# Optimization experiments

Hardware: AMD Instinct MI355X
Metric: run time of the kernel (lower is better)

Reference implementation:

```python
import jax, jax.numpy as jnp
import numpy as np

B, C, L = 32, 128, 4096          # batch, n_channels, signal length
P, Q = 100, 20                   # n_projections, n_quantiles


def setup_inputs() -> dict:
    key = jax.random.key(0)
    k1, k2, k3, k4 = jax.random.split(key, 4)
    X = jax.random.normal(k1, (B, C, L), dtype=jnp.float32)
    # conv1d kernel of shape (P, C, 1) collapsed to (P, C)
    W = jax.random.normal(k2, (P, C), dtype=jnp.float32)
    s = 2.33 * jnp.sqrt(jnp.float32(C))
    min_vals = -s + 0.1 * jax.random.normal(k3, (P,), dtype=jnp.float32)
    max_vals = s + 0.1 * jax.random.normal(k4, (P,), dtype=jnp.float32)
    return {"X": X, "W": W, "min_vals": min_vals, "max_vals": max_vals}


def reference(X, W, min_vals, max_vals):
    # kernel-size-1 conv1d == channel projection
    a = jnp.einsum('bcl,pc->bpl', X, W)  # [B, P, L]
    fracs = jnp.arange(1, Q + 1, dtype=a.dtype) / jnp.asarray(Q + 1, a.dtype)
    thr = min_vals[None, :] + (max_vals - min_vals)[None, :] * fracs[:, None]  # [Q, P]

    def body(carry, t):  # t: [P] thresholds for one quantile
        cdf_q = jnp.mean((a < t[None, :, None]).astype(a.dtype), axis=-1)  # [B, P]
        return carry, cdf_q

    _, cdf = jax.lax.scan(body, None, thr)          # [Q, B, P]
    cdf = jnp.transpose(cdf, (1, 2, 0))             # [B, P, Q]
    return cdf.reshape(B, P * Q)
```

## Files before the change

kernel.cpp:

```cpp
#include <hip/hip_runtime.h>
#include <hip/hip_bf16.h>

#define B_    32
#define C_    128
#define L_    4096
#define P_    100
#define NPT   7
#define Q_    20
#define NBIN  21
#define HSTR  37
#define NCH   (NPT * 4)
#define CHS   512
#define TPB   1024
#define LSPAN 512

typedef short          bf16x8 __attribute__((ext_vector_type(8)));
typedef float          f32x4  __attribute__((ext_vector_type(4)));
typedef unsigned short u16x8  __attribute__((ext_vector_type(8)));

__device__ inline unsigned short f2bf(float f) {
    __hip_bfloat16 h = __float2bfloat16(f);
    unsigned short u; __builtin_memcpy(&u, &h, 2);
    return u;
}

__global__ void prep_w_kernel(const float* __restrict__ W, unsigned short* __restrict__ Wf) {
    const int t = blockIdx.x * 256 + threadIdx.x;
    if (t >= NCH * 64) return;
    const int chunk = t >> 6, lane = t & 63;
    const int pt = chunk >> 2, ks = chunk & 3;
    const int p  = pt * 16 + (lane & 15);
    const int c0 = ks * 32 + (lane >> 4) * 8;
    u16x8 v;
#pragma unroll
    for (int j = 0; j < 8; ++j)
        v[j] = (p < P_) ? f2bf(W[p * C_ + c0 + j]) : (unsigned short)0;
    *(u16x8*)(Wf + (size_t)t * 8) = v;
}

__global__ __launch_bounds__(TPB, 4)
void radon_mfma8_kernel(const float* __restrict__ X, const unsigned short* __restrict__ Wf,
                        const float* __restrict__ minv, const float* __restrict__ maxv,
                        float* __restrict__ out) {
    __shared__ unsigned short Wlds[NCH * CHS];
    __shared__ int   hist[P_ * HSTR];
    __shared__ float mn_s[P_], invd_s[P_];

    const int tid  = threadIdx.x;
    const int b    = blockIdx.y;
    const int lblk = blockIdx.x;
    const int wave = tid >> 6;
    const int lane = tid & 63;
    const int quad = lane >> 4;
    const int nn   = lane & 15;

    {
        const int4* src = (const int4*)Wf;
        int4* dst = (int4*)Wlds;
        for (int k = tid; k < NCH * 64; k += TPB)
            dst[k] = src[k];
    }
    for (int i = tid; i < P_; i += TPB) {
        const float mn = minv[i];
        mn_s[i]   = mn;
        invd_s[i] = (float)NBIN / (maxv[i] - mn);
    }
    for (int i = tid; i < P_ * HSTR; i += TPB) hist[i] = 0;
    __syncthreads();

    const int l0 = lblk * LSPAN + wave * 32;
    const float* Xb = X + (size_t)b * C_ * L_;
    float xv[2][4][8];
#pragma unroll
    for (int lt = 0; lt < 2; ++lt)
#pragma unroll
        for (int ks = 0; ks < 4; ++ks)
#pragma unroll
            for (int j = 0; j < 8; ++j)
                xv[lt][ks][j] = Xb[(size_t)(ks * 32 + quad * 8 + j) * L_ + l0 + lt * 16 + nn];

    bf16x8 bfrag[2][4];
#pragma unroll
    for (int lt = 0; lt < 2; ++lt)
#pragma unroll
        for (int ks = 0; ks < 4; ++ks) {
            unsigned int u[4];
#pragma unroll
            for (int jp = 0; jp < 4; ++jp) {
                __hip_bfloat162 h2 = __float22bfloat162_rn(
                    make_float2(xv[lt][ks][2 * jp], xv[lt][ks][2 * jp + 1]));
                __builtin_memcpy(&u[jp], &h2, 4);
            }
            __builtin_memcpy(&bfrag[lt][ks], u, 16);
        }

    for (int pt = 0; pt < NPT; ++pt) {
        bf16x8 afrag[4];
#pragma unroll
        for (int ks = 0; ks < 4; ++ks)
            afrag[ks] = *(const bf16x8*)(&Wlds[((pt * 4 + ks) * 64 + lane) * 8]);

        f32x4 acc0 = {0.f, 0.f, 0.f, 0.f};
        f32x4 acc1 = {0.f, 0.f, 0.f, 0.f};
#pragma unroll
        for (int ks = 0; ks < 4; ++ks) {
            acc0 = __builtin_amdgcn_mfma_f32_16x16x32_bf16(bfrag[0][ks], afrag[ks], acc0, 0, 0, 0);
            acc1 = __builtin_amdgcn_mfma_f32_16x16x32_bf16(bfrag[1][ks], afrag[ks], acc1, 0, 0, 0);
        }

        const int p = pt * 16 + nn;
        if (p < P_) {
            const float mn = mn_s[p], invd = invd_s[p];
            int* __restrict__ hrow = &hist[p * HSTR];
#pragma unroll
            for (int r = 0; r < 4; ++r) {
                {
                    const float t = (acc0[r] - mn) * invd;
                    int k = 0;
                    if (t > 0.f) { const int ki = (int)t; k = (ki > 20) ? 20 : ki; }
                    atomicAdd(&hrow[k], 1);
                }
                {
                    const float t = (acc1[r] - mn) * invd;
                    int k = 0;
                    if (t > 0.f) { const int ki = (int)t; k = (ki > 20) ? 20 : ki; }
                    atomicAdd(&hrow[k], 1);
                }
            }
        }
    }
    __syncthreads();

    if (tid < P_) {
        int* row = &hist[tid * HSTR];
        int run = 0;
#pragma unroll
        for (int k = 0; k < NBIN; ++k) { run += row[k]; row[k] = run; }
    }
    __syncthreads();

    for (int i = tid; i < P_ * Q_; i += TPB) {
        const int p  = i / Q_;
        const int qi = i - p * Q_;
        const int s  = hist[p * HSTR + qi];
        atomicAdd(&out[((size_t)b * P_ + p) * Q_ + qi], (float)s * (1.0f / (float)L_));
    }
}

extern "C" void kernel_launch(void* const* d_in, const int* in_sizes, int n_in,
                              void* d_out, int out_size, void* d_ws, size_t ws_size,
                              hipStream_t stream) {
    const float* X  = (const float*)d_in[0];
    const float* W  = (const float*)d_in[1];
    const float* mn = (const float*)d_in[2];
    const float* mx = (const float*)d_in[3];
    float* out = (float*)d_out;
    unsigned short* Wf = (unsigned short*)d_ws;

    hipMemsetAsync(out, 0, (size_t)out_size * sizeof(float), stream);
    prep_w_kernel<<<NCH * 64 / 256, 256, 0, stream>>>(W, Wf);

    dim3 grid(L_ / LSPAN, B_);
    radon_mfma8_kernel<<<grid, dim3(TPB), 0, stream>>>(X, Wf, mn, mx, out);
}
```

Before: 104.1 us.

## Widen per-wave L tile to 64 with float4 loads and double-buffered channel chunks

Each wave now covers 64 signal positions instead of 32. It loads X as float4 vectors and double-buffers the channel chunks so the next chunk's global loads overlap the MFMAs on the current one. All projection-tile accumulators (7x4) stay in registers, and each W fragment is read from LDS once per K-step and reused across four column tiles. The block is halved to 512 threads so each block still spans 512 positions. The aim is fewer, wider memory transactions, better latency hiding, and more reuse of A fragments, at the cost of much higher register pressure and lower occupancy.

```diff
diff --git a/kernel.cpp b/kernel.cpp
--- a/kernel.cpp
+++ b/kernel.cpp
@@ -11,7 +11,7 @@
 #define HSTR  37
 #define NCH   (NPT * 4)
 #define CHS   512
-#define TPB   1024
+#define TPB   512
 #define LSPAN 512
 
 typedef short          bf16x8 __attribute__((ext_vector_type(8)));
@@ -38,10 +38,10 @@
     *(u16x8*)(Wf + (size_t)t * 8) = v;
 }
 
-__global__ __launch_bounds__(TPB, 4)
-void radon_mfma8_kernel(const float* __restrict__ X, const unsigned short* __restrict__ Wf,
-                        const float* __restrict__ minv, const float* __restrict__ maxv,
-                        float* __restrict__ out) {
+__global__ __launch_bounds__(TPB, 2)
+void radon_mfma10_kernel(const float* __restrict__ X, const unsigned short* __restrict__ Wf,
+                         const float* __restrict__ minv, const float* __restrict__ maxv,
+                         float* __restrict__ out) {
     __shared__ unsigned short Wlds[NCH * CHS];
     __shared__ int   hist[P_ * HSTR];
     __shared__ float mn_s[P_], invd_s[P_];
@@ -68,65 +68,67 @@
     for (int i = tid; i < P_ * HSTR; i += TPB) hist[i] = 0;
     __syncthreads();
 
-    const int l0 = lblk * LSPAN + wave * 32;
-    const float* Xb = X + (size_t)b * C_ * L_;
-    float xv[2][4][8];
+    const int l0 = lblk * LSPAN + wave * 64;
+    const float* Xb = X + (size_t)b * C_ * L_ + l0 + 4 * nn;
+
+    f32x4 acc[NPT][4];
 #pragma unroll
-    for (int lt = 0; lt < 2; ++lt)
+    for (int pt = 0; pt < NPT; ++pt)
 #pragma unroll
-        for (int ks = 0; ks < 4; ++ks)
+        for (int t = 0; t < 4; ++t)
+            acc[pt][t] = (f32x4){0.f, 0.f, 0.f, 0.f};
+
+    float4 xf[2][8];
+#pragma unroll
+    for (int j = 0; j < 8; ++j)
+        xf[0][j] = *(const float4*)(Xb + (size_t)(quad * 8 + j) * L_);
+
+#pragma unroll
+    for (int ks = 0; ks < 4; ++ks) {
+        __builtin_amdgcn_sched_barrier(0);
+        const int cur = ks & 1, nxt = cur ^ 1;
+        if (ks < 3) {
 #pragma unroll
             for (int j = 0; j < 8; ++j)
-                xv[lt][ks][j] = Xb[(size_t)(ks * 32 + quad * 8 + j) * L_ + l0 + lt * 16 + nn];
-
-    bf16x8 bfrag[2][4];
+                xf[nxt][j] = *(const float4*)(Xb + (size_t)((ks + 1) * 32 + quad * 8 + j) * L_);
+        }
+        bf16x8 bt[4];
 #pragma unroll
-    for (int lt = 0; lt < 2; ++lt)
-#pragma unroll
-        for (int ks = 0; ks < 4; ++ks) {
+        for (int t = 0; t < 4; ++t) {
             unsigned int u[4];
 #pragma unroll
             for (int jp = 0; jp < 4; ++jp) {
-                __hip_bfloat162 h2 = __float22bfloat162_rn(
-                    make_float2(xv[lt][ks][2 * jp], xv[lt][ks][2 * jp + 1]));
+                const float lo = ((const float*)&xf[cur][2 * jp])[t];
+                const float hi = ((const float*)&xf[cur][2 * jp + 1])[t];
+                __hip_bfloat162 h2 = __float22bfloat162_rn(make_float2(lo, hi));
                 __builtin_memcpy(&u[jp], &h2, 4);
             }
-            __builtin_memcpy(&bfrag[lt][ks], u, 16);
+            __builtin_memcpy(&bt[t], u, 16);
         }
+#pragma unroll
+        for (int pt = 0; pt < NPT; ++pt) {
+            bf16x8 a = *(const bf16x8*)(&Wlds[((pt * 4 + ks) * 64 + lane) * 8]);
+#pragma unroll
+            for (int t = 0; t < 4; ++t)
+                acc[pt][t] = __builtin_amdgcn_mfma_f32_16x16x32_bf16(bt[t], a, acc[pt][t], 0, 0, 0);
+        }
+    }
 
+#pragma unroll
     for (int pt = 0; pt < NPT; ++pt) {
-        bf16x8 afrag[4];
-#pragma unroll
-        for (int ks = 0; ks < 4; ++ks)
-            afrag[ks] = *(const bf16x8*)(&Wlds[((pt * 4 + ks) * 64 + lane) * 8]);
-
-        f32x4 acc0 = {0.f, 0.f, 0.f, 0.f};
-        f32x4 acc1 = {0.f, 0.f, 0.f, 0.f};
-#pragma unroll
-        for (int ks = 0; ks < 4; ++ks) {
-            acc0 = __builtin_amdgcn_mfma_f32_16x16x32_bf16(bfrag[0][ks], afrag[ks], acc0, 0, 0, 0);
-            acc1 = __builtin_amdgcn_mfma_f32_16x16x32_bf16(bfrag[1][ks], afrag[ks], acc1, 0, 0, 0);
-        }
-
         const int p = pt * 16 + nn;
         if (p < P_) {
             const float mn = mn_s[p], invd = invd_s[p];
             int* __restrict__ hrow = &hist[p * HSTR];
 #pragma unroll
-            for (int r = 0; r < 4; ++r) {
-                {
-                    const float t = (acc0[r] - mn) * invd;
+            for (int t = 0; t < 4; ++t)
+#pragma unroll
+                for (int r = 0; r < 4; ++r) {
+                    const float tt = (acc[pt][t][r] - mn) * invd;
                     int k = 0;
-                    if (t > 0.f) { const int ki = (int)t; k = (ki > 20) ? 20 : ki; }
+                    if (tt > 0.f) { const int ki = (int)tt; k = (ki > 20) ? 20 : ki; }
                     atomicAdd(&hrow[k], 1);
                 }
-                {
-                    const float t = (acc1[r] - mn) * invd;
-                    int k = 0;
-                    if (t > 0.f) { const int ki = (int)t; k = (ki > 20) ? 20 : ki; }
-                    atomicAdd(&hrow[k], 1);
-                }
-            }
         }
     }
     __syncthreads();
@@ -161,5 +163,5 @@
     prep_w_kernel<<<NCH * 64 / 256, 256, 0, stream>>>(W, Wf);
 
     dim3 grid(L_ / LSPAN, B_);
-    radon_mfma8_kernel<<<grid, dim3(TPB), 0, stream>>>(X, Wf, mn, mx, out);
+    radon_mfma10_kernel<<<grid, dim3(TPB), 0, stream>>>(X, Wf, mn, mx, out);
 }
```

Result: no change. 104.7 us (+0.6%).
